# Optimization experiments

Measured on AMD Instinct MI355X. Metric: run time of the kernel, lower is better.

## Reference

```python
import jax, jax.numpy as jnp
import numpy as np

NUM_EXPERTS = 8
TOP_K = 2
BALANCE_LOSS_COEF = 0.01


def setup_inputs() -> dict:
    key = jax.random.key(0)
    ks = jax.random.split(key, 5)
    B, S, H, I, E = 8, 2048, 512, 2048, NUM_EXPERTS
    return {
        "hidden_states": jax.random.normal(ks[0], (B, S, H), dtype=jnp.float32),
        "Wg": jax.random.normal(ks[1], (H, E), dtype=jnp.float32) * (1.0 / np.sqrt(H)),
        "bg": jnp.zeros((E,), dtype=jnp.float32),
        "W1": jax.random.normal(ks[2], (E, H, I), dtype=jnp.float32) * (1.0 / np.sqrt(H)),
        "b1": jnp.zeros((E, I), dtype=jnp.float32),
        "W2": jax.random.normal(ks[3], (E, I, H), dtype=jnp.float32) * (1.0 / np.sqrt(I)),
        "b2": jnp.zeros((E, H), dtype=jnp.float32),
    }


def reference(hidden_states, Wg, bg, W1, b1, W2, b2):
    B, S, H = hidden_states.shape
    E, K = NUM_EXPERTS, TOP_K

    # ---- Router: softmax gate + top-k, renormalized weights ----
    logits = jnp.einsum('bsh,he->bse', hidden_states, Wg) + bg       # [B,S,E]
    probs = jax.nn.softmax(logits, axis=-1)                          # [B,S,E]
    top_p, top_i = jax.lax.top_k(probs, K)                           # [B,S,K]
    routing_weights = top_p / jnp.sum(top_p, axis=-1, keepdims=True)  # [B,S,K]

    # ---- Experts: compute every expert densely (small fixed E), then gather ----
    h = jnp.einsum('bsh,ehi->ebsi', hidden_states, W1) + b1[:, None, None, :]
    h = jax.nn.gelu(h)
    y = jnp.einsum('ebsi,eih->ebsh', h, W2) + b2[:, None, None, :]   # [E,B,S,H]

    y = jnp.moveaxis(y, 0, 2)                                        # [B,S,E,H]
    sel = jnp.take_along_axis(y, top_i[..., None], axis=2)           # [B,S,K,H]
    output = jnp.sum(routing_weights[..., None] * sel, axis=2) + hidden_states

    # ---- Load balancing loss (Switch-style): E * sum_e f_e * P_e ----
    assign = jnp.sum(jax.nn.one_hot(top_i, E, dtype=probs.dtype), axis=2)  # [B,S,E]
    f = jnp.mean(assign, axis=(0, 1)) / K                            # fraction dispatched
    P = jnp.mean(probs, axis=(0, 1))                                 # mean router prob
    balance_loss = BALANCE_LOSS_COEF * E * jnp.sum(f * P)

    return output, balance_loss
```

## Files before the change

### kernel.cpp

```cpp
#include <hip/hip_runtime.h>

#define BS_TOK 16384
#define HD 512
#define IDIM 2048
#define NE 8
#define RT_MAX 264
#define CAP (RT_MAX * 128)

typedef unsigned short u16;
typedef unsigned int u32;
typedef unsigned long long u64;
typedef __attribute__((ext_vector_type(8))) __bf16 bf16x8;
typedef __attribute__((ext_vector_type(4))) float f32x4;

__device__ __forceinline__ u16 f2bf(float f) {
  u32 u = __builtin_bit_cast(u32, f);
  u += 0x7fffu + ((u >> 16) & 1u);
  return (u16)(u >> 16);
}
__device__ __forceinline__ u16 f2bf_hw(float f) {
  u32 r;
  asm("v_cvt_pk_bf16_f32 %0, %1, %2" : "=v"(r) : "v"(f), "v"(f));
  return (u16)r;
}
__device__ __forceinline__ u32 pack2bf(float a, float b) {
  u32 r;
  asm("v_cvt_pk_bf16_f32 %0, %1, %2" : "=v"(r) : "v"(a), "v"(b));
  return r;
}
__device__ __forceinline__ float bflo(u32 u) { return __builtin_bit_cast(float, u << 16); }
__device__ __forceinline__ float bfhi(u32 u) { return __builtin_bit_cast(float, u & 0xffff0000u); }
__device__ __forceinline__ float gelu_t(float v) {
  float t = v * (-2.302558f - 0.1029474f * v * v);
  return v * __builtin_amdgcn_rcpf(1.0f + __builtin_amdgcn_exp2f(t));
}
__device__ __forceinline__ void gload16(const u16* g, u16* l) {
  __builtin_amdgcn_global_load_lds((const __attribute__((address_space(1))) u16*)g,
                                   (__attribute__((address_space(3))) u16*)l, 16, 0, 0);
}

__global__ void k_prep(const float* __restrict__ W1, u16* __restrict__ W1T,
                       const float* __restrict__ W2, u16* __restrict__ W2T,
                       const float* __restrict__ x, const float* __restrict__ Wg,
                       const float* __restrict__ bg, int* __restrict__ top_e,
                       float* __restrict__ top_w, u32* __restrict__ counts,
                       float* __restrict__ Psum, u16* __restrict__ xb) {
  __shared__ float t[64][65];
  __shared__ float wg_s[HD * 9];
  __shared__ float Pp[NE];
  __shared__ u32 cnt[NE];
  int bid = blockIdx.x;
  int tid = threadIdx.x;
  if (bid < 4096) {
    int z = bid >> 8, tl = bid & 255;
    const float* in; u16* out; int Rin, Cin;
    if (z < NE) { in = W1; out = W1T; Rin = HD; Cin = IDIM; }
    else { in = W2; out = W2T; Rin = IDIM; Cin = HD; z -= NE; }
    size_t eb = (size_t)z * HD * IDIM;
    int tpr = Cin >> 6;
    int r0 = (tl / tpr) << 6, c0 = (tl % tpr) << 6;
    int row = tid >> 4, c4 = (tid & 15) << 2;
    #pragma unroll
    for (int i = 0; i < 4; ++i) {
      float4 v = *(const float4*)(in + eb + (size_t)(r0 + row + i * 16) * Cin + c0 + c4);
      t[row + i * 16][c4 + 0] = v.x; t[row + i * 16][c4 + 1] = v.y;
      t[row + i * 16][c4 + 2] = v.z; t[row + i * 16][c4 + 3] = v.w;
    }
    __syncthreads();
    int cc = tid >> 4, rr = (tid & 15) << 2;
    #pragma unroll
    for (int i = 0; i < 4; ++i) {
      int c = cc + i * 16;
      u32 lo = pack2bf(t[rr + 0][c], t[rr + 1][c]);
      u32 hi = pack2bf(t[rr + 2][c], t[rr + 3][c]);
      u64 v = (u64)lo | ((u64)hi << 32);
      *(u64*)(out + eb + (size_t)(c0 + c) * Rin + r0 + rr) = v;
    }
    return;
  }
  if (tid < NE) { Pp[tid] = 0.f; cnt[tid] = 0; }
  for (int i = tid; i < HD * NE; i += 256) wg_s[(i >> 3) * 9 + (i & 7)] = Wg[i];
  __syncthreads();
  int wv = tid >> 6, lane = tid & 63;
  int tk = (bid - 4096) * 4 + wv;

  const float4* xr = (const float4*)(x + (size_t)tk * HD + lane * 8);
  float4 a = xr[0], b = xr[1];
  u32 p0 = pack2bf(a.x, a.y), p1 = pack2bf(a.z, a.w);
  u32 p2 = pack2bf(b.x, b.y), p3 = pack2bf(b.z, b.w);
  ((uint4*)(xb + (size_t)tk * HD))[lane] = make_uint4(p0, p1, p2, p3);

  float acc[NE];
  #pragma unroll
  for (int e = 0; e < NE; ++e) acc[e] = 0.f;
  #pragma unroll
  for (int j = 0; j < 8; ++j) {
    int h = lane + 64 * j;
    float xv = x[(size_t)tk * HD + h];
    const float* wrow = wg_s + h * 9;
    #pragma unroll
    for (int e = 0; e < NE; ++e) acc[e] += xv * wrow[e];
  }
  #pragma unroll
  for (int off = 32; off > 0; off >>= 1) {
    #pragma unroll
    for (int e = 0; e < NE; ++e) acc[e] += __shfl_down(acc[e], off);
  }
  if (lane == 0) {
    float lg[NE];
    #pragma unroll
    for (int e = 0; e < NE; ++e) lg[e] = acc[e] + bg[e];
    int i1 = 0; float m1 = lg[0];
    #pragma unroll
    for (int e = 1; e < NE; ++e) if (lg[e] > m1) { m1 = lg[e]; i1 = e; }
    int i2 = -1; float m2 = -1e30f;
    #pragma unroll
    for (int e = 0; e < NE; ++e) if (e != i1 && lg[e] > m2) { m2 = lg[e]; i2 = e; }
    float s = 0.f, p[NE];
    #pragma unroll
    for (int e = 0; e < NE; ++e) { p[e] = __expf(lg[e] - m1); s += p[e]; }
    float inv = 1.f / s;
    #pragma unroll
    for (int e = 0; e < NE; ++e) { p[e] *= inv; atomicAdd(&Pp[e], p[e]); }
    float denom = p[i1] + p[i2];
    top_e[2 * tk] = i1; top_e[2 * tk + 1] = i2;
    top_w[2 * tk] = p[i1] / denom; top_w[2 * tk + 1] = p[i2] / denom;
    atomicAdd(&cnt[i1], 1u); atomicAdd(&cnt[i2], 1u);
  }
  __syncthreads();
  if (tid < NE) { atomicAdd(&counts[tid], cnt[tid]); atomicAdd(&Psum[tid], Pp[tid]); }
}

__global__ void k_scatter(const int* __restrict__ top_e, const float* __restrict__ top_w,
                          const u32* __restrict__ counts, const float* __restrict__ Psum,
                          u32* __restrict__ pos_rel, int* __restrict__ perm_t,
                          u32* __restrict__ padoff, float* __restrict__ out) {
  __shared__ u32 po[NE];
  if (threadIdx.x == 0) {
    u32 off = 0; float loss = 0.f;
    for (int e = 0; e < NE; ++e) {
      po[e] = off;
      off += ((counts[e] + 127u) / 128u) * 128u;
      loss += ((float)counts[e] / (float)(BS_TOK * 2)) * (Psum[e] / (float)BS_TOK);
    }
    if (blockIdx.x == 0) {
      for (int e = 0; e < NE; ++e) padoff[e] = po[e];
      padoff[NE] = off;
      out[(size_t)BS_TOK * HD] = 0.01f * (float)NE * loss;
    }
  }
  __syncthreads();
  int g = blockIdx.x * 256 + threadIdx.x;
  int e = top_e[g];
  int lane = threadIdx.x & 63;
  #pragma unroll
  for (int ee = 0; ee < NE; ++ee) {
    unsigned long long m = __ballot(e == ee);
    if (e == ee) {
      int nb = __popcll(m & ((1ull << lane) - 1ull));
      int leader = __ffsll((unsigned long long)m) - 1;
      u32 base = 0;
      if (lane == leader) base = atomicAdd(&pos_rel[ee], (u32)__popcll(m));
      base = __shfl(base, leader);
      int slot = (int)(po[ee] + base) + nb;
      perm_t[slot] = g;
    }
  }
}

template <int KSTEPS, int NCT, int NTOT, bool GATHER, bool ACT, bool SCAT>
__global__ __launch_bounds__(256, 2) void k_gemm(
    const u16* __restrict__ A, int lda, const u16* __restrict__ W,
    const float* __restrict__ bias, const int* __restrict__ perm_t,
    const u32* __restrict__ padoff, u16* __restrict__ C) {
  __shared__ u16 As[2][8192], Bs[2][8192];
  int nb = gridDim.x;
  int b = blockIdx.x;
  int tile = (b & 7) * (nb >> 3) + (b >> 3);
  int rt = tile / NCT, ct = tile % NCT;
  u32 s0 = (u32)rt * 128u;
  if (s0 >= padoff[NE]) return;
  int e = 0;
  #pragma unroll
  for (int k = 1; k < NE; ++k) e += (s0 >= padoff[k]) ? 1 : 0;

  int tid = threadIdx.x;
  int wv = tid >> 6, lane = tid & 63;
  int l15 = lane & 15, lg4 = lane >> 4;
  int wr = wv >> 1, wc = wv & 1;

  int srow = tid >> 3;
  int cb = (tid & 7) * 16;
  int cbs = (cb ^ ((srow & 7) << 4)) >> 1;

  const u16* ap[4]; const u16* bp[4];
  #pragma unroll
  for (int i = 0; i < 4; ++i) {
    int r = i * 32 + srow;
    int arow;
    if (GATHER) {
      int g = perm_t[s0 + r];
      arow = (g < 0 ? 0 : g) >> 1;
    } else {
      arow = (int)(s0 + r);
    }
    ap[i] = A + (size_t)arow * lda + cbs;
    bp[i] = W + ((size_t)e * NTOT + ct * 128 + r) * (KSTEPS * 64) + cbs;
  }

  int base_n = ct * 128 + wc * 64;
  f32x4 acc[4][4];
  #pragma unroll
  for (int j = 0; j < 4; ++j) {
    float bv = bias[e * NTOT + base_n + j * 16 + l15];
    #pragma unroll
    for (int i = 0; i < 4; ++i) acc[i][j] = f32x4{bv, bv, bv, bv};
  }

  #pragma unroll
  for (int i = 0; i < 4; ++i) gload16(ap[i], As[0] + tid * 8 + i * 2048);
  #pragma unroll
  for (int i = 0; i < 4; ++i) gload16(bp[i], Bs[0] + tid * 8 + i * 2048);
  #pragma unroll
  for (int i = 0; i < 4; ++i) gload16(ap[i] + 64, As[1] + tid * 8 + i * 2048);
  #pragma unroll
  for (int i = 0; i < 4; ++i) gload16(bp[i] + 64, Bs[1] + tid * 8 + i * 2048);
  asm volatile("s_waitcnt vmcnt(8)" ::: "memory");
  __builtin_amdgcn_sched_barrier(0);
  __builtin_amdgcn_s_barrier();

  for (int ks = 0; ks < KSTEPS; ++ks) {
    int cur = ks & 1;
    const u16* Ab = As[cur];
    const u16* Bb = Bs[cur];
    bf16x8 af[2][4], bf[2][4];
    #pragma unroll
    for (int kk = 0; kk < 2; ++kk) {
      #pragma unroll
      for (int f = 0; f < 4; ++f) {
        int ra = wr * 64 + f * 16 + l15;
        af[kk][f] = *(const bf16x8*)((const char*)Ab +
                    (ra * 128 + ((kk * 64 + lg4 * 16) ^ ((ra & 7) << 4))));
        int rb = wc * 64 + f * 16 + l15;
        bf[kk][f] = *(const bf16x8*)((const char*)Bb +
                    (rb * 128 + ((kk * 64 + lg4 * 16) ^ ((rb & 7) << 4))));
      }
    }
    asm volatile("s_waitcnt lgkmcnt(0)" ::: "memory");
    __builtin_amdgcn_sched_barrier(0);
    __builtin_amdgcn_s_barrier();

    if (ks + 2 < KSTEPS) {
      int k0 = (ks + 2) * 64;
      #pragma unroll
      for (int i = 0; i < 4; ++i) gload16(ap[i] + k0, As[cur] + tid * 8 + i * 2048);
      #pragma unroll
      for (int i = 0; i < 4; ++i) gload16(bp[i] + k0, Bs[cur] + tid * 8 + i * 2048);
    }

    __builtin_amdgcn_s_setprio(1);
    #pragma unroll
    for (int kk = 0; kk < 2; ++kk)
      #pragma unroll
      for (int i = 0; i < 4; ++i)
        #pragma unroll
        for (int j = 0; j < 4; ++j)
          acc[i][j] = __builtin_amdgcn_mfma_f32_16x16x32_bf16(af[kk][i], bf[kk][j], acc[i][j], 0, 0, 0);
    __builtin_amdgcn_s_setprio(0);

    if (ks + 1 < KSTEPS) {
      if (ks + 2 < KSTEPS) {
        asm volatile("s_waitcnt vmcnt(8)" ::: "memory");
      } else {
        asm volatile("s_waitcnt vmcnt(0)" ::: "memory");
      }
      __builtin_amdgcn_sched_barrier(0);
      __builtin_amdgcn_s_barrier();
    }
  }

  #pragma unroll
  for (int i = 0; i < 4; ++i) {
    u32 mrow = s0 + wr * 64 + i * 16 + lg4 * 4;
    #pragma unroll
    for (int rr = 0; rr < 4; ++rr) {
      u32 m = mrow + rr;
      if (SCAT) {
        int g = perm_t[m];
        if (g >= 0) {
          #pragma unroll
          for (int j = 0; j < 4; ++j)
            C[(size_t)g * NTOT + base_n + j * 16 + l15] = f2bf_hw(acc[i][j][rr]);
        }
      } else {
        #pragma unroll
        for (int j = 0; j < 4; ++j) {
          float v = acc[i][j][rr];
          if (ACT) v = gelu_t(v);
          C[(size_t)m * NTOT + base_n + j * 16 + l15] = f2bf_hw(v);
        }
      }
    }
  }
}

__global__ void k_final(const float* __restrict__ x, const u16* __restrict__ y2,
                        const float* __restrict__ top_w, float* __restrict__ out) {
  int tid = threadIdx.x;
  int t = blockIdx.x * 4 + (tid >> 6);
  int lane = tid & 63;
  float w0 = top_w[2 * t], w1 = top_w[2 * t + 1];
  size_t xo = (size_t)t * HD + lane * 8;
  float4 a = *(const float4*)(x + xo);
  float4 b = *(const float4*)(x + xo + 4);
  uint4 ya = *(const uint4*)(y2 + (size_t)(2 * t) * HD + lane * 8);
  uint4 yb = *(const uint4*)(y2 + (size_t)(2 * t + 1) * HD + lane * 8);
  float4 o0, o1;
  o0.x = a.x + w0 * bflo(ya.x) + w1 * bflo(yb.x);
  o0.y = a.y + w0 * bfhi(ya.x) + w1 * bfhi(yb.x);
  o0.z = a.z + w0 * bflo(ya.y) + w1 * bflo(yb.y);
  o0.w = a.w + w0 * bfhi(ya.y) + w1 * bfhi(yb.y);
  o1.x = b.x + w0 * bflo(ya.z) + w1 * bflo(yb.z);
  o1.y = b.y + w0 * bfhi(ya.z) + w1 * bfhi(yb.z);
  o1.z = b.z + w0 * bflo(ya.w) + w1 * bflo(yb.w);
  o1.w = b.w + w0 * bfhi(ya.w) + w1 * bfhi(yb.w);
  *(float4*)(out + xo) = o0;
  *(float4*)(out + xo + 4) = o1;
}

extern "C" void kernel_launch(void* const* d_in, const int* in_sizes, int n_in,
                              void* d_out, int out_size, void* d_ws, size_t ws_size,
                              hipStream_t stream) {
  const float* x  = (const float*)d_in[0];
  const float* Wg = (const float*)d_in[1];
  const float* bg = (const float*)d_in[2];
  const float* W1 = (const float*)d_in[3];
  const float* b1 = (const float*)d_in[4];
  const float* W2 = (const float*)d_in[5];
  const float* b2 = (const float*)d_in[6];
  float* out = (float*)d_out;

  char* w = (char*)d_ws;
  u32* counts   = (u32*)(w + 0);
  u32* pos_rel  = (u32*)(w + 32);
  float* Psum   = (float*)(w + 64);
  u32* padoff   = (u32*)(w + 96);
  int* perm_t   = (int*)(w + 256);
  int* top_e    = (int*)(w + 135424);
  float* top_w  = (float*)(w + 266496);
  u16* xb  = (u16*)(w + 397568);
  u16* W1T = (u16*)(w + 17174784);
  u16* W2T = (u16*)(w + 33952000);
  u16* h   = (u16*)(w + 50729216);
  u16* y2  = (u16*)(w + 189141248);
  if (ws_size < 224010496ull) return;

  (void)hipMemsetAsync(w, 0, 256, stream);
  (void)hipMemsetAsync(w + 256, 0xFF, 135168, stream);
  k_prep<<<8192, 256, 0, stream>>>(W1, W1T, W2, W2T, x, Wg, bg,
                                   top_e, top_w, counts, Psum, xb);
  k_scatter<<<(BS_TOK * 2) / 256, 256, 0, stream>>>(top_e, top_w, counts, Psum,
                                                    pos_rel, perm_t, padoff, out);
  k_gemm<8, 16, IDIM, true, true, false><<<RT_MAX * 16, 256, 0, stream>>>(
      xb, HD, W1T, b1, perm_t, padoff, h);
  k_gemm<32, 4, HD, false, false, true><<<RT_MAX * 4, 256, 0, stream>>>(
      h, IDIM, W2T, b2, perm_t, padoff, y2);
  k_final<<<BS_TOK / 4, 256, 0, stream>>>(x, y2, top_w, out);
}
```

Before: 342.2 us.

## Widen GEMM tiles to 128x256 with 512 threads and triple-buffered LDS

Moves the expert GEMMs from 128x128 tiles with 4 waves to 128x256 tiles with 8 waves, so each A tile is reused across twice as many output columns. The LDS ring grows from two to three stages, which lets the next prefetch be issued before the current fragments are read and drops one barrier per k-step. It also replaces the memset of the padding slots in perm_t with in-kernel fills of only the padded tails in the scatter kernel. In exchange, LDS use rises to about 144KB per block and the grids shrink, which may reduce occupancy and the number of blocks per CU. The race safety of the single-barrier, three-slot scheme relies on the barrier ordering.

Result: slower. 396.0 us (+15.7%).

```diff
diff --git a/kernel.cpp b/kernel.cpp
--- a/kernel.cpp
+++ b/kernel.cpp
@@ -150,6 +150,14 @@
     }
   }
   __syncthreads();
+  if (blockIdx.x == 0) {
+    #pragma unroll
+    for (int e = 0; e < NE; ++e) {
+      u32 c = counts[e];
+      u32 pc = ((c + 127u) / 128u) * 128u;
+      for (u32 i = c + threadIdx.x; i < pc; i += 256) perm_t[po[e] + i] = -1;
+    }
+  }
   int g = blockIdx.x * 256 + threadIdx.x;
   int e = top_e[g];
   int lane = threadIdx.x & 63;
@@ -169,11 +177,12 @@
 }
 
 template <int KSTEPS, int NCT, int NTOT, bool GATHER, bool ACT, bool SCAT>
-__global__ __launch_bounds__(256, 2) void k_gemm(
+__global__ __launch_bounds__(512, 2) void k_gemm(
     const u16* __restrict__ A, int lda, const u16* __restrict__ W,
     const float* __restrict__ bias, const int* __restrict__ perm_t,
     const u32* __restrict__ padoff, u16* __restrict__ C) {
-  __shared__ u16 As[2][8192], Bs[2][8192];
+  __shared__ u16 As[3][8192];
+  __shared__ u16 Bs[3][16384];
   int nb = gridDim.x;
   int b = blockIdx.x;
   int tile = (b & 7) * (nb >> 3) + (b >> 3);
@@ -187,101 +196,100 @@
   int tid = threadIdx.x;
   int wv = tid >> 6, lane = tid & 63;
   int l15 = lane & 15, lg4 = lane >> 4;
-  int wr = wv >> 1, wc = wv & 1;
-
-  int srow = tid >> 3;
+  int wm = wv >> 2, wn = wv & 3;
+
   int cb = (tid & 7) * 16;
-  int cbs = (cb ^ ((srow & 7) << 4)) >> 1;
-
-  const u16* ap[4]; const u16* bp[4];
-  #pragma unroll
-  for (int i = 0; i < 4; ++i) {
-    int r = i * 32 + srow;
+  const u16* ap[2]; const u16* bp[4];
+  #pragma unroll
+  for (int i = 0; i < 2; ++i) {
+    int row = (tid >> 3) + i * 64;
+    int off = (cb ^ ((row & 7) << 4)) >> 1;
     int arow;
     if (GATHER) {
-      int g = perm_t[s0 + r];
+      int g = perm_t[s0 + row];
       arow = (g < 0 ? 0 : g) >> 1;
     } else {
-      arow = (int)(s0 + r);
-    }
-    ap[i] = A + (size_t)arow * lda + cbs;
-    bp[i] = W + ((size_t)e * NTOT + ct * 128 + r) * (KSTEPS * 64) + cbs;
-  }
-
-  int base_n = ct * 128 + wc * 64;
+      arow = (int)(s0 + row);
+    }
+    ap[i] = A + (size_t)arow * lda + off;
+  }
+  #pragma unroll
+  for (int i = 0; i < 4; ++i) {
+    int row = (tid >> 3) + i * 64;
+    int off = (cb ^ ((row & 7) << 4)) >> 1;
+    bp[i] = W + ((size_t)e * NTOT + ct * 256 + row) * (KSTEPS * 64) + off;
+  }
+
+  int base_n = ct * 256 + wn * 64;
   f32x4 acc[4][4];
   #pragma unroll
-  for (int j = 0; j < 4; ++j) {
-    float bv = bias[e * NTOT + base_n + j * 16 + l15];
-    #pragma unroll
-    for (int i = 0; i < 4; ++i) acc[i][j] = f32x4{bv, bv, bv, bv};
-  }
-
-  #pragma unroll
-  for (int i = 0; i < 4; ++i) gload16(ap[i], As[0] + tid * 8 + i * 2048);
-  #pragma unroll
-  for (int i = 0; i < 4; ++i) gload16(bp[i], Bs[0] + tid * 8 + i * 2048);
-  #pragma unroll
-  for (int i = 0; i < 4; ++i) gload16(ap[i] + 64, As[1] + tid * 8 + i * 2048);
-  #pragma unroll
-  for (int i = 0; i < 4; ++i) gload16(bp[i] + 64, Bs[1] + tid * 8 + i * 2048);
-  asm volatile("s_waitcnt vmcnt(8)" ::: "memory");
-  __builtin_amdgcn_sched_barrier(0);
+  for (int fc = 0; fc < 4; ++fc) {
+    float bv = bias[(size_t)e * NTOT + base_n + fc * 16 + l15];
+    #pragma unroll
+    for (int fr = 0; fr < 4; ++fr) acc[fr][fc] = f32x4{bv, bv, bv, bv};
+  }
+
+  #pragma unroll
+  for (int i = 0; i < 2; ++i) gload16(ap[i], As[0] + tid * 8 + i * 4096);
+  #pragma unroll
+  for (int i = 0; i < 4; ++i) gload16(bp[i], Bs[0] + tid * 8 + i * 4096);
+  #pragma unroll
+  for (int i = 0; i < 2; ++i) gload16(ap[i] + 64, As[1] + tid * 8 + i * 4096);
+  #pragma unroll
+  for (int i = 0; i < 4; ++i) gload16(bp[i] + 64, Bs[1] + tid * 8 + i * 4096);
+  asm volatile("s_waitcnt vmcnt(6)" ::: "memory");
   __builtin_amdgcn_s_barrier();
+  asm volatile("" ::: "memory");
 
   for (int ks = 0; ks < KSTEPS; ++ks) {
-    int cur = ks & 1;
-    const u16* Ab = As[cur];
-    const u16* Bb = Bs[cur];
+    int slot = ks % 3;
+    if (ks + 2 < KSTEPS) {
+      int sl2 = (ks + 2) % 3;
+      int k0 = (ks + 2) * 64;
+      #pragma unroll
+      for (int i = 0; i < 2; ++i) gload16(ap[i] + k0, As[sl2] + tid * 8 + i * 4096);
+      #pragma unroll
+      for (int i = 0; i < 4; ++i) gload16(bp[i] + k0, Bs[sl2] + tid * 8 + i * 4096);
+    }
+    const u16* Ab = As[slot];
+    const u16* Bb = Bs[slot];
     bf16x8 af[2][4], bf[2][4];
     #pragma unroll
     for (int kk = 0; kk < 2; ++kk) {
       #pragma unroll
       for (int f = 0; f < 4; ++f) {
-        int ra = wr * 64 + f * 16 + l15;
+        int ra = wm * 64 + f * 16 + l15;
         af[kk][f] = *(const bf16x8*)((const char*)Ab +
                     (ra * 128 + ((kk * 64 + lg4 * 16) ^ ((ra & 7) << 4))));
-        int rb = wc * 64 + f * 16 + l15;
+        int rb = wn * 64 + f * 16 + l15;
         bf[kk][f] = *(const bf16x8*)((const char*)Bb +
                     (rb * 128 + ((kk * 64 + lg4 * 16) ^ ((rb & 7) << 4))));
       }
     }
-    asm volatile("s_waitcnt lgkmcnt(0)" ::: "memory");
-    __builtin_amdgcn_sched_barrier(0);
-    __builtin_amdgcn_s_barrier();
-
-    if (ks + 2 < KSTEPS) {
-      int k0 = (ks + 2) * 64;
-      #pragma unroll
-      for (int i = 0; i < 4; ++i) gload16(ap[i] + k0, As[cur] + tid * 8 + i * 2048);
-      #pragma unroll
-      for (int i = 0; i < 4; ++i) gload16(bp[i] + k0, Bs[cur] + tid * 8 + i * 2048);
-    }
-
     __builtin_amdgcn_s_setprio(1);
     #pragma unroll
     for (int kk = 0; kk < 2; ++kk)
       #pragma unroll
-      for (int i = 0; i < 4; ++i)
+      for (int fr = 0; fr < 4; ++fr)
         #pragma unroll
-        for (int j = 0; j < 4; ++j)
-          acc[i][j] = __builtin_amdgcn_mfma_f32_16x16x32_bf16(af[kk][i], bf[kk][j], acc[i][j], 0, 0, 0);
+        for (int fc = 0; fc < 4; ++fc)
+          acc[fr][fc] = __builtin_amdgcn_mfma_f32_16x16x32_bf16(af[kk][fr], bf[kk][fc], acc[fr][fc], 0, 0, 0);
     __builtin_amdgcn_s_setprio(0);
 
     if (ks + 1 < KSTEPS) {
       if (ks + 2 < KSTEPS) {
-        asm volatile("s_waitcnt vmcnt(8)" ::: "memory");
+        asm volatile("s_waitcnt vmcnt(6)" ::: "memory");
       } else {
         asm volatile("s_waitcnt vmcnt(0)" ::: "memory");
       }
-      __builtin_amdgcn_sched_barrier(0);
       __builtin_amdgcn_s_barrier();
-    }
-  }
-
-  #pragma unroll
-  for (int i = 0; i < 4; ++i) {
-    u32 mrow = s0 + wr * 64 + i * 16 + lg4 * 4;
+      asm volatile("" ::: "memory");
+    }
+  }
+
+  #pragma unroll
+  for (int fr = 0; fr < 4; ++fr) {
+    u32 mrow = s0 + wm * 64 + fr * 16 + lg4 * 4;
     #pragma unroll
     for (int rr = 0; rr < 4; ++rr) {
       u32 m = mrow + rr;
@@ -289,15 +297,15 @@
         int g = perm_t[m];
         if (g >= 0) {
           #pragma unroll
-          for (int j = 0; j < 4; ++j)
-            C[(size_t)g * NTOT + base_n + j * 16 + l15] = f2bf_hw(acc[i][j][rr]);
+          for (int fc = 0; fc < 4; ++fc)
+            C[(size_t)g * NTOT + base_n + fc * 16 + l15] = f2bf_hw(acc[fr][fc][rr]);
         }
       } else {
         #pragma unroll
-        for (int j = 0; j < 4; ++j) {
-          float v = acc[i][j][rr];
+        for (int fc = 0; fc < 4; ++fc) {
+          float v = acc[fr][fc][rr];
           if (ACT) v = gelu_t(v);
-          C[(size_t)m * NTOT + base_n + j * 16 + l15] = f2bf_hw(v);
+          C[(size_t)m * NTOT + base_n + fc * 16 + l15] = f2bf_hw(v);
         }
       }
     }
@@ -356,14 +364,13 @@
   if (ws_size < 224010496ull) return;
 
   (void)hipMemsetAsync(w, 0, 256, stream);
-  (void)hipMemsetAsync(w + 256, 0xFF, 135168, stream);
   k_prep<<<8192, 256, 0, stream>>>(W1, W1T, W2, W2T, x, Wg, bg,
                                    top_e, top_w, counts, Psum, xb);
   k_scatter<<<(BS_TOK * 2) / 256, 256, 0, stream>>>(top_e, top_w, counts, Psum,
                                                     pos_rel, perm_t, padoff, out);
-  k_gemm<8, 16, IDIM, true, true, false><<<RT_MAX * 16, 256, 0, stream>>>(
+  k_gemm<8, 8, IDIM, true, true, false><<<RT_MAX * 8, 512, 0, stream>>>(
       xb, HD, W1T, b1, perm_t, padoff, h);
-  k_gemm<32, 4, HD, false, false, true><<<RT_MAX * 4, 256, 0, stream>>>(
+  k_gemm<32, 2, HD, false, false, true><<<RT_MAX * 2, 512, 0, stream>>>(
       h, IDIM, W2T, b2, perm_t, padoff, y2);
   k_final<<<BS_TOK / 4, 256, 0, stream>>>(x, y2, top_w, out);
 }
```

## Use 256x256 tiles with 8 waves for the first expert GEMM

Applied to the files above, without the earlier changes.

Replaces the templated first GEMM with a dedicated 512-thread kernel that computes 256x256 output tiles, each wave owning a 128x64 sub-tile, with MFMA work interleaved with prefetch loads. Expert segments are padded to 256 rows, and k_scatter now fills the padding slots with -1 in place of a separate memset. The y2 buffer reuses the xb storage to shrink the workspace. The aim is more data reuse per loaded tile and less global traffic in the large up-projection GEMM. The cost is more padding waste, higher register and LDS pressure, and fewer blocks in flight.

New measurement: 352.2 us. 1.03x slower.

```diff
diff --git a/kernel.cpp b/kernel.cpp
--- a/kernel.cpp
+++ b/kernel.cpp
@@ -4,8 +4,9 @@
 #define HD 512
 #define IDIM 2048
 #define NE 8
-#define RT_MAX 264
-#define CAP (RT_MAX * 128)
+#define RT256 136
+#define RT128 (RT256 * 2)
+#define CAP (RT256 * 256)
 
 typedef unsigned short u16;
 typedef unsigned int u32;
@@ -140,7 +141,7 @@
     u32 off = 0; float loss = 0.f;
     for (int e = 0; e < NE; ++e) {
       po[e] = off;
-      off += ((counts[e] + 127u) / 128u) * 128u;
+      off += ((counts[e] + 255u) / 256u) * 256u;
       loss += ((float)counts[e] / (float)(BS_TOK * 2)) * (Psum[e] / (float)BS_TOK);
     }
     if (blockIdx.x == 0) {
@@ -150,6 +151,14 @@
     }
   }
   __syncthreads();
+  if (blockIdx.x == 0) {
+    #pragma unroll
+    for (int e = 0; e < NE; ++e) {
+      u32 c = counts[e];
+      u32 pc = ((c + 255u) / 256u) * 256u;
+      for (u32 i = c + threadIdx.x; i < pc; i += 256) perm_t[po[e] + i] = -1;
+    }
+  }
   int g = blockIdx.x * 256 + threadIdx.x;
   int e = top_e[g];
   int lane = threadIdx.x & 63;
@@ -168,8 +177,159 @@
   }
 }
 
-template <int KSTEPS, int NCT, int NTOT, bool GATHER, bool ACT, bool SCAT>
-__global__ __launch_bounds__(256, 2) void k_gemm(
+__global__ __launch_bounds__(512, 2) void k_gemm1(
+    const u16* __restrict__ xb, const u16* __restrict__ W1T,
+    const float* __restrict__ bias, const int* __restrict__ perm_t,
+    const u32* __restrict__ padoff, u16* __restrict__ h) {
+  __shared__ u16 As[2][16384], Bs[2][16384];
+  int nb = gridDim.x;
+  int b = blockIdx.x;
+  int tile = (b & 7) * (nb >> 3) + (b >> 3);
+  int rt = tile >> 3, ct = tile & 7;
+  u32 s0 = (u32)rt * 256u;
+  if (s0 >= padoff[NE]) return;
+  int e = 0;
+  #pragma unroll
+  for (int k = 1; k < NE; ++k) e += (s0 >= padoff[k]) ? 1 : 0;
+
+  int tid = threadIdx.x;
+  int wv = tid >> 6, lane = tid & 63;
+  int l15 = lane & 15, lg4 = lane >> 4;
+  int wm = wv >> 2, wn = wv & 3;
+
+  const u16* apg[4]; const u16* bpg[4];
+  #pragma unroll
+  for (int i = 0; i < 4; ++i) {
+    int row = (tid >> 3) + i * 64;
+    int off = (((tid & 7) * 16) ^ ((row & 7) << 4)) >> 1;
+    int g = perm_t[s0 + row];
+    apg[i] = xb + (size_t)((g < 0 ? 0 : g) >> 1) * HD + off;
+    bpg[i] = W1T + ((size_t)e * IDIM + ct * 256 + row) * HD + off;
+  }
+
+  int base_n = ct * 256 + wn * 64;
+  f32x4 acc[8][4];
+  #pragma unroll
+  for (int fc = 0; fc < 4; ++fc) {
+    float bv = bias[(size_t)e * IDIM + base_n + fc * 16 + l15];
+    #pragma unroll
+    for (int fr = 0; fr < 8; ++fr) acc[fr][fc] = f32x4{bv, bv, bv, bv};
+  }
+
+  #pragma unroll
+  for (int i = 0; i < 4; ++i) gload16(apg[i], As[0] + tid * 8 + i * 4096);
+  #pragma unroll
+  for (int i = 0; i < 4; ++i) gload16(bpg[i], Bs[0] + tid * 8 + i * 4096);
+  #pragma unroll
+  for (int i = 0; i < 4; ++i) gload16(apg[i] + 64, As[1] + tid * 8 + i * 4096);
+  #pragma unroll
+  for (int i = 0; i < 4; ++i) gload16(bpg[i] + 64, Bs[1] + tid * 8 + i * 4096);
+  asm volatile("s_waitcnt vmcnt(8)" ::: "memory");
+  __builtin_amdgcn_sched_barrier(0);
+  __builtin_amdgcn_s_barrier();
+
+  #define LDFRAG(BUF, ROW, KK) \
+    *(const bf16x8*)((const char*)(BUF) + ((ROW) * 128 + (((KK) * 64 + lg4 * 16) ^ (((ROW) & 7) << 4))))
+
+  for (int t = 0; t < 8; ++t) {
+    int buf = t & 1;
+    const u16* Ab = As[buf];
+    const u16* Bb = Bs[buf];
+    u16* Ad = As[buf];
+    u16* Bd = Bs[buf];
+    int k0 = (t + 2) * 64;
+    bool pf = (t + 2) < 8;
+
+    bf16x8 af[2][4], bfr[2][4];
+    #pragma unroll
+    for (int kk = 0; kk < 2; ++kk) {
+      #pragma unroll
+      for (int f = 0; f < 4; ++f) af[kk][f] = LDFRAG(Ab, wm * 128 + f * 16 + l15, kk);
+      #pragma unroll
+      for (int c = 0; c < 4; ++c) bfr[kk][c] = LDFRAG(Bb, wn * 64 + c * 16 + l15, kk);
+    }
+    asm volatile("s_waitcnt lgkmcnt(0)" ::: "memory");
+    __builtin_amdgcn_sched_barrier(0);
+    __builtin_amdgcn_s_barrier();
+    __builtin_amdgcn_s_setprio(1);
+    #pragma unroll
+    for (int kk = 0; kk < 2; ++kk)
+      #pragma unroll
+      for (int f = 0; f < 4; ++f)
+        #pragma unroll
+        for (int c = 0; c < 2; ++c)
+          acc[f][c] = __builtin_amdgcn_mfma_f32_16x16x32_bf16(af[kk][f], bfr[kk][c], acc[f][c], 0, 0, 0);
+    __builtin_amdgcn_s_setprio(0);
+
+    if (pf) {
+      #pragma unroll
+      for (int i = 0; i < 4; ++i) gload16(bpg[i] + k0, Bd + tid * 8 + i * 4096);
+    }
+    __builtin_amdgcn_s_setprio(1);
+    #pragma unroll
+    for (int kk = 0; kk < 2; ++kk)
+      #pragma unroll
+      for (int f = 0; f < 4; ++f)
+        #pragma unroll
+        for (int c = 2; c < 4; ++c)
+          acc[f][c] = __builtin_amdgcn_mfma_f32_16x16x32_bf16(af[kk][f], bfr[kk][c], acc[f][c], 0, 0, 0);
+    __builtin_amdgcn_s_setprio(0);
+
+    #pragma unroll
+    for (int kk = 0; kk < 2; ++kk)
+      #pragma unroll
+      for (int f = 0; f < 4; ++f) af[kk][f] = LDFRAG(Ab, wm * 128 + 64 + f * 16 + l15, kk);
+    asm volatile("s_waitcnt lgkmcnt(0)" ::: "memory");
+    __builtin_amdgcn_sched_barrier(0);
+    __builtin_amdgcn_s_barrier();
+    __builtin_amdgcn_s_setprio(1);
+    #pragma unroll
+    for (int kk = 0; kk < 2; ++kk)
+      #pragma unroll
+      for (int f = 0; f < 4; ++f)
+        #pragma unroll
+        for (int c = 0; c < 2; ++c)
+          acc[4 + f][c] = __builtin_amdgcn_mfma_f32_16x16x32_bf16(af[kk][f], bfr[kk][c], acc[4 + f][c], 0, 0, 0);
+    __builtin_amdgcn_s_setprio(0);
+
+    if (pf) {
+      #pragma unroll
+      for (int i = 0; i < 4; ++i) gload16(apg[i] + k0, Ad + tid * 8 + i * 4096);
+    }
+    if (t + 1 < 8) {
+      if (pf) asm volatile("s_waitcnt vmcnt(8)" ::: "memory");
+      else    asm volatile("s_waitcnt vmcnt(0)" ::: "memory");
+      __builtin_amdgcn_sched_barrier(0);
+      __builtin_amdgcn_s_barrier();
+    }
+    __builtin_amdgcn_s_setprio(1);
+    #pragma unroll
+    for (int kk = 0; kk < 2; ++kk)
+      #pragma unroll
+      for (int f = 0; f < 4; ++f)
+        #pragma unroll
+        for (int c = 2; c < 4; ++c)
+          acc[4 + f][c] = __builtin_amdgcn_mfma_f32_16x16x32_bf16(af[kk][f], bfr[kk][c], acc[4 + f][c], 0, 0, 0);
+    __builtin_amdgcn_s_setprio(0);
+  }
+  #undef LDFRAG
+
+  #pragma unroll
+  for (int fr = 0; fr < 8; ++fr) {
+    u32 mrow = s0 + wm * 128 + fr * 16 + lg4 * 4;
+    #pragma unroll
+    for (int rr = 0; rr < 4; ++rr) {
+      #pragma unroll
+      for (int fc = 0; fc < 4; ++fc) {
+        float v = gelu_t(acc[fr][fc][rr]);
+        h[(size_t)(mrow + rr) * IDIM + base_n + fc * 16 + l15] = f2bf_hw(v);
+      }
+    }
+  }
+}
+
+template <int KSTEPS, int NCT, int NTOT>
+__global__ __launch_bounds__(256, 2) void k_gemm2(
     const u16* __restrict__ A, int lda, const u16* __restrict__ W,
     const float* __restrict__ bias, const int* __restrict__ perm_t,
     const u32* __restrict__ padoff, u16* __restrict__ C) {
@@ -197,14 +357,7 @@
   #pragma unroll
   for (int i = 0; i < 4; ++i) {
     int r = i * 32 + srow;
-    int arow;
-    if (GATHER) {
-      int g = perm_t[s0 + r];
-      arow = (g < 0 ? 0 : g) >> 1;
-    } else {
-      arow = (int)(s0 + r);
-    }
-    ap[i] = A + (size_t)arow * lda + cbs;
+    ap[i] = A + (size_t)(s0 + r) * lda + cbs;
     bp[i] = W + ((size_t)e * NTOT + ct * 128 + r) * (KSTEPS * 64) + cbs;
   }
 
@@ -284,21 +437,11 @@
     u32 mrow = s0 + wr * 64 + i * 16 + lg4 * 4;
     #pragma unroll
     for (int rr = 0; rr < 4; ++rr) {
-      u32 m = mrow + rr;
-      if (SCAT) {
-        int g = perm_t[m];
-        if (g >= 0) {
-          #pragma unroll
-          for (int j = 0; j < 4; ++j)
-            C[(size_t)g * NTOT + base_n + j * 16 + l15] = f2bf_hw(acc[i][j][rr]);
-        }
-      } else {
+      int g = perm_t[mrow + rr];
+      if (g >= 0) {
         #pragma unroll
-        for (int j = 0; j < 4; ++j) {
-          float v = acc[i][j][rr];
-          if (ACT) v = gelu_t(v);
-          C[(size_t)m * NTOT + base_n + j * 16 + l15] = f2bf_hw(v);
-        }
+        for (int j = 0; j < 4; ++j)
+          C[(size_t)g * NTOT + base_n + j * 16 + l15] = f2bf_hw(acc[i][j][rr]);
       }
     }
   }
@@ -346,24 +489,21 @@
   float* Psum   = (float*)(w + 64);
   u32* padoff   = (u32*)(w + 96);
   int* perm_t   = (int*)(w + 256);
-  int* top_e    = (int*)(w + 135424);
-  float* top_w  = (float*)(w + 266496);
-  u16* xb  = (u16*)(w + 397568);
-  u16* W1T = (u16*)(w + 17174784);
-  u16* W2T = (u16*)(w + 33952000);
-  u16* h   = (u16*)(w + 50729216);
-  u16* y2  = (u16*)(w + 189141248);
-  if (ws_size < 224010496ull) return;
+  int* top_e    = (int*)(w + 139520);
+  float* top_w  = (float*)(w + 270592);
+  u16* xb  = (u16*)(w + 401664);
+  u16* W1T = (u16*)(w + 17178880);
+  u16* W2T = (u16*)(w + 33956096);
+  u16* h   = (u16*)(w + 50733312);
+  u16* y2  = xb;
+  if (ws_size < 193339648ull) return;
 
   (void)hipMemsetAsync(w, 0, 256, stream);
-  (void)hipMemsetAsync(w + 256, 0xFF, 135168, stream);
   k_prep<<<8192, 256, 0, stream>>>(W1, W1T, W2, W2T, x, Wg, bg,
                                    top_e, top_w, counts, Psum, xb);
   k_scatter<<<(BS_TOK * 2) / 256, 256, 0, stream>>>(top_e, top_w, counts, Psum,
                                                     pos_rel, perm_t, padoff, out);
-  k_gemm<8, 16, IDIM, true, true, false><<<RT_MAX * 16, 256, 0, stream>>>(
-      xb, HD, W1T, b1, perm_t, padoff, h);
-  k_gemm<32, 4, HD, false, false, true><<<RT_MAX * 4, 256, 0, stream>>>(
-      h, IDIM, W2T, b2, perm_t, padoff, y2);
+  k_gemm1<<<RT256 * 8, 512, 0, stream>>>(xb, W1T, b1, perm_t, padoff, h);
+  k_gemm2<32, 4, HD><<<RT128 * 4, 256, 0, stream>>>(h, IDIM, W2T, b2, perm_t, padoff, y2);
   k_final<<<BS_TOK / 4, 256, 0, stream>>>(x, y2, top_w, out);
 }
```
